# Kernel tuning notes

Hardware: AMD Instinct MI355X
Metric: run time of the kernel (lower is better)

Reference implementation:

```python
import jax, jax.numpy as jnp
import numpy as np

ALPHA = 0.2          # LeakyReLU negative slope (args.alpha)
NEG_INF = -9e15      # zero_vec constant from the torch source


def _build_mask(neighbors):
    """Faithful port of A_creat: scatter-add edge counts, row-normalize,
    add self-loops (identity), row-normalize again. neighbors: [N, deg] int."""
    N, deg = neighbors.shape
    rows = jnp.repeat(jnp.arange(N), deg)
    counts = jnp.zeros((N, N), jnp.float32).at[rows, neighbors.reshape(-1)].add(1.0)
    m = counts / counts.sum(axis=1, keepdims=True)
    m = m + jnp.eye(N, dtype=jnp.float32)
    m = m / m.sum(axis=1, keepdims=True)
    return m


def setup_inputs() -> dict:
    key = jax.random.key(0)
    k1, k2, k3, k4 = jax.random.split(key, 4)
    N, F_IN, F_OUT, DEG = 8192, 256, 128, 32
    h = jax.random.normal(k1, (N, F_IN), dtype=jnp.float32)
    neighbors = jax.random.randint(k2, (N, DEG), 0, N)
    # torch uses nn.init.uniform_ (U[0,1)) for both W and a
    W = jax.random.uniform(k3, (F_IN, F_OUT), dtype=jnp.float32)
    a = jax.random.uniform(k4, (2 * F_OUT, 1), dtype=jnp.float32)
    return {"h": h, "W": W, "a": a, "neighbors": neighbors}


def reference(h, W, a, neighbors):
    F_out = W.shape[1]
    mask = _build_mask(neighbors)                 # [N, N]
    hW = h @ W                                    # [N, F_out]
    h1 = hW @ a[:F_out]                           # [N, 1]
    h2 = hW @ a[F_out:]                           # [N, 1]
    e = mask * (h1 + h2.T)                        # dense masked additive scores
    e = jnp.where(e > 0, e, ALPHA * e)            # LeakyReLU
    att = jnp.where(e != 0.0, e, NEG_INF)         # mask out zeros
    att = jax.nn.softmax(att, axis=1)             # row softmax (dropout off in eval)
    feat = att @ hW                               # aggregate
    return jax.nn.elu(feat)
```

## Files before the change

### kernel.cpp

```cpp
#include <hip/hip_runtime.h>
#include <math.h>

#define N_NODES 8192
#define F_IN    256
#define F_OUT   128
#define DEG     32
#define ALPHA   0.2f

__global__ void gemm_hw_kernel(const float* __restrict__ h,
                               const float* __restrict__ W,
                               float* __restrict__ hW) {
    __shared__ float hs[8 * F_IN];
    const int tid  = threadIdx.x;
    const int row0 = blockIdx.x * 8;

    const float4* hsrc = (const float4*)(h + (size_t)row0 * F_IN);
    float4* hdst = (float4*)hs;
    #pragma unroll
    for (int t = 0; t < 4; ++t)
        hdst[tid + t * 128] = hsrc[tid + t * 128];
    __syncthreads();

    float acc[8] = {0.f, 0.f, 0.f, 0.f, 0.f, 0.f, 0.f, 0.f};
    #pragma unroll 4
    for (int k = 0; k < F_IN; ++k) {
        float w = W[k * F_OUT + tid];
        #pragma unroll
        for (int r = 0; r < 8; ++r)
            acc[r] = fmaf(hs[r * F_IN + k], w, acc[r]);
    }
    #pragma unroll
    for (int r = 0; r < 8; ++r)
        hW[(size_t)(row0 + r) * F_OUT + tid] = acc[r];
}

__global__ void h1h2_kernel(const float* __restrict__ hW,
                            const float* __restrict__ a,
                            float* __restrict__ h1,
                            float* __restrict__ h2) {
    const int wave = threadIdx.x >> 6;
    const int lane = threadIdx.x & 63;
    const int row  = blockIdx.x * 4 + wave;
    const float* hr = hW + (size_t)row * F_OUT;

    float s1 = 0.f, s2 = 0.f;
    #pragma unroll
    for (int j = lane; j < F_OUT; j += 64) {
        float v = hr[j];
        s1 = fmaf(v, a[j], s1);
        s2 = fmaf(v, a[F_OUT + j], s2);
    }
    #pragma unroll
    for (int off = 32; off > 0; off >>= 1) {
        s1 += __shfl_down(s1, off);
        s2 += __shfl_down(s2, off);
    }
    if (lane == 0) { h1[row] = s1; h2[row] = s2; }
}

__global__ void attn_kernel(const float* __restrict__ hW,
                            const float* __restrict__ h1,
                            const float* __restrict__ h2,
                            const int*   __restrict__ nbr,
                            float* __restrict__ out) {
    const int wave = threadIdx.x >> 6;
    const int lane = threadIdx.x & 63;
    const int row  = blockIdx.x * 4 + wave;

    int col = -1;
    if (lane < DEG)       col = nbr[(size_t)row * DEG + lane];
    else if (lane == DEG) col = row;

    int cnt = 0;
    int firstq = lane;
    #pragma unroll
    for (int q = 0; q <= DEG; ++q) {
        int cq = __shfl(col, q);
        bool same = (cq == col);
        if (same && q < DEG)    cnt++;
        if (same && q < firstq) firstq = q;
    }
    const bool active = (lane <= DEG) && (col >= 0) && (firstq == lane);

    float mask_val = (float)cnt * (1.0f / 64.0f) + ((col == row) ? 0.5f : 0.0f);

    const float h1row = h1[row];
    float h2c = active ? h2[col] : 0.f;
    float s = mask_val * (h1row + h2c);
    float e = (s > 0.f) ? s : ALPHA * s;
    bool valid = active && (e != 0.0f);

    float ev = valid ? e : -INFINITY;
    #pragma unroll
    for (int off = 32; off > 0; off >>= 1)
        ev = fmaxf(ev, __shfl_xor(ev, off));
    float w = valid ? expf(e - ev) : 0.f;
    float denom = w;
    #pragma unroll
    for (int off = 32; off > 0; off >>= 1)
        denom += __shfl_xor(denom, off);
    float att = w / denom;

    float acc0 = 0.f, acc1 = 0.f;
    #pragma unroll
    for (int q = 0; q <= DEG; ++q) {
        float aq = __shfl(att, q);
        int   cq = __shfl(col, q);
        if (aq > 0.f) {
            const float* hr = hW + (size_t)cq * F_OUT;
            acc0 = fmaf(aq, hr[lane],      acc0);
            acc1 = fmaf(aq, hr[64 + lane], acc1);
        }
    }

    float o0 = (acc0 > 0.f) ? acc0 : expm1f(acc0);
    float o1 = (acc1 > 0.f) ? acc1 : expm1f(acc1);
    out[(size_t)row * F_OUT + lane]      = o0;
    out[(size_t)row * F_OUT + 64 + lane] = o1;
}

extern "C" void kernel_launch(void* const* d_in, const int* in_sizes, int n_in,
                              void* d_out, int out_size, void* d_ws, size_t ws_size,
                              hipStream_t stream) {
    const float* h   = (const float*)d_in[0];
    const float* W   = (const float*)d_in[1];
    const float* a   = (const float*)d_in[2];
    const int*   nbr = (const int*)  d_in[3];
    float* out = (float*)d_out;

    float* hW = (float*)d_ws;
    float* h1 = hW + (size_t)N_NODES * F_OUT;
    float* h2 = h1 + N_NODES;

    gemm_hw_kernel<<<N_NODES / 8, 128, 0, stream>>>(h, W, hW);
    h1h2_kernel   <<<N_NODES / 4, 256, 0, stream>>>(hW, a, h1, h2);
    attn_kernel   <<<N_NODES / 4, 256, 0, stream>>>(hW, h1, h2, nbr, out);
}
```

Before: 102.8 us.

## Fuse attention-vector dot into a register-tiled GEMM and store hW as bf16

Replaces the naive hW GEMM with a 16-row register-tiled kernel. It double-buffers its LDS tiles, loading W asynchronously straight into LDS and staging h through registers. The h1/h2 projections are folded into the GEMM epilogue, which removes a separate kernel launch and a re-read of hW. hW is written as packed bf16 pairs, halving the gather traffic in the attention kernel, which also switches to fast __expf and vectorized float2 output stores. In exchange, the aggregated features lose precision because of the bf16 hW, and the GEMM grows more complex.

```diff
diff --git a/kernel.cpp b/kernel.cpp
--- a/kernel.cpp
+++ b/kernel.cpp
@@ -7,62 +7,133 @@
 #define DEG     32
 #define ALPHA   0.2f
 
-__global__ void gemm_hw_kernel(const float* __restrict__ h,
-                               const float* __restrict__ W,
-                               float* __restrict__ hW) {
-    __shared__ float hs[8 * F_IN];
+#define BR      16
+#define KC      32
+#define HP      36
+#define NCHUNK  (F_IN / KC)
+
+typedef const uint32_t __attribute__((address_space(1)))* gas_ptr;
+typedef uint32_t __attribute__((address_space(3)))* las_ptr;
+
+__device__ __forceinline__ void async_copy16(const float* g, float* l) {
+    __builtin_amdgcn_global_load_lds((gas_ptr)g, (las_ptr)l, 16, 0, 0);
+}
+
+__device__ __forceinline__ unsigned short f2bf(float x) {
+    unsigned u = __float_as_uint(x);
+    return (unsigned short)((u + 0x7fffu + ((u >> 16) & 1u)) >> 16);
+}
+
+__global__ __launch_bounds__(256) void gemm_fused_v4(
+        const float* __restrict__ h,
+        const float* __restrict__ W,
+        const float* __restrict__ a,
+        unsigned int* __restrict__ hWb,
+        float* __restrict__ h1,
+        float* __restrict__ h2) {
+    __shared__ float hT[2][BR * HP];
+    __shared__ float wT[2][KC * F_OUT];
+
     const int tid  = threadIdx.x;
-    const int row0 = blockIdx.x * 8;
-
-    const float4* hsrc = (const float4*)(h + (size_t)row0 * F_IN);
-    float4* hdst = (float4*)hs;
-    #pragma unroll
-    for (int t = 0; t < 4; ++t)
-        hdst[tid + t * 128] = hsrc[tid + t * 128];
+    const int wv   = tid >> 6;
+    const int lane = tid & 63;
+    const int cg   = tid & 31;
+    const int rg   = tid >> 5;
+    const int c0   = cg * 4;
+    const int r0   = rg * 2;
+    const int row0 = blockIdx.x * BR;
+
+    float acc[2][4] = {{0.f,0.f,0.f,0.f},{0.f,0.f,0.f,0.f}};
+
+    auto stage_w = [&](int k0, int buf) {
+        const float* gsrc = W + (size_t)k0 * F_OUT + wv * 1024 + lane * 4;
+        float*       ldst = wT[buf] + wv * 1024;
+        #pragma unroll
+        for (int it = 0; it < 4; ++it)
+            async_copy16(gsrc + it * 256, ldst + it * 256);
+    };
+    const int hrow = tid >> 3;
+    const int hkq  = (tid & 7) * 4;
+    auto load_h = [&](int k0) -> float4 {
+        if (tid < 128)
+            return *(const float4*)(h + (size_t)(row0 + hrow) * F_IN + k0 + hkq);
+        return make_float4(0.f, 0.f, 0.f, 0.f);
+    };
+    auto commit_h = [&](float4 v, int buf) {
+        if (tid < 128)
+            *(float4*)(hT[buf] + hrow * HP + hkq) = v;
+    };
+
+    stage_w(0, 0);
+    commit_h(load_h(0), 0);
     __syncthreads();
 
-    float acc[8] = {0.f, 0.f, 0.f, 0.f, 0.f, 0.f, 0.f, 0.f};
-    #pragma unroll 4
-    for (int k = 0; k < F_IN; ++k) {
-        float w = W[k * F_OUT + tid];
+    for (int ch = 0; ch < NCHUNK; ++ch) {
+        const int cur = ch & 1, nxt = cur ^ 1;
+        float4 hv_next;
+        if (ch + 1 < NCHUNK) {
+            stage_w((ch + 1) * KC, nxt);
+            hv_next = load_h((ch + 1) * KC);
+        }
+
+        const float* hc = hT[cur];
+        const float* wc = wT[cur];
         #pragma unroll
-        for (int r = 0; r < 8; ++r)
-            acc[r] = fmaf(hs[r * F_IN + k], w, acc[r]);
-    }
-    #pragma unroll
-    for (int r = 0; r < 8; ++r)
-        hW[(size_t)(row0 + r) * F_OUT + tid] = acc[r];
-}
-
-__global__ void h1h2_kernel(const float* __restrict__ hW,
-                            const float* __restrict__ a,
-                            float* __restrict__ h1,
-                            float* __restrict__ h2) {
-    const int wave = threadIdx.x >> 6;
-    const int lane = threadIdx.x & 63;
-    const int row  = blockIdx.x * 4 + wave;
-    const float* hr = hW + (size_t)row * F_OUT;
-
-    float s1 = 0.f, s2 = 0.f;
-    #pragma unroll
-    for (int j = lane; j < F_OUT; j += 64) {
-        float v = hr[j];
-        s1 = fmaf(v, a[j], s1);
-        s2 = fmaf(v, a[F_OUT + j], s2);
-    }
-    #pragma unroll
-    for (int off = 32; off > 0; off >>= 1) {
-        s1 += __shfl_down(s1, off);
-        s2 += __shfl_down(s2, off);
-    }
-    if (lane == 0) { h1[row] = s1; h2[row] = s2; }
-}
-
-__global__ void attn_kernel(const float* __restrict__ hW,
-                            const float* __restrict__ h1,
-                            const float* __restrict__ h2,
-                            const int*   __restrict__ nbr,
-                            float* __restrict__ out) {
+        for (int k4 = 0; k4 < KC; k4 += 4) {
+            float4 h0 = *(const float4*)(hc + (r0    ) * HP + k4);
+            float4 h1v= *(const float4*)(hc + (r0 + 1) * HP + k4);
+            const float h0a[4] = {h0.x, h0.y, h0.z, h0.w};
+            const float h1a[4] = {h1v.x, h1v.y, h1v.z, h1v.w};
+            #pragma unroll
+            for (int kk = 0; kk < 4; ++kk) {
+                float4 wvv = *(const float4*)(wc + (k4 + kk) * F_OUT + c0);
+                acc[0][0] = fmaf(h0a[kk], wvv.x, acc[0][0]);
+                acc[0][1] = fmaf(h0a[kk], wvv.y, acc[0][1]);
+                acc[0][2] = fmaf(h0a[kk], wvv.z, acc[0][2]);
+                acc[0][3] = fmaf(h0a[kk], wvv.w, acc[0][3]);
+                acc[1][0] = fmaf(h1a[kk], wvv.x, acc[1][0]);
+                acc[1][1] = fmaf(h1a[kk], wvv.y, acc[1][1]);
+                acc[1][2] = fmaf(h1a[kk], wvv.z, acc[1][2]);
+                acc[1][3] = fmaf(h1a[kk], wvv.w, acc[1][3]);
+            }
+        }
+
+        if (ch + 1 < NCHUNK) commit_h(hv_next, nxt);
+        __syncthreads();
+    }
+
+    #pragma unroll
+    for (int i = 0; i < 2; ++i) {
+        uint2 p;
+        p.x = (unsigned)f2bf(acc[i][0]) | ((unsigned)f2bf(acc[i][1]) << 16);
+        p.y = (unsigned)f2bf(acc[i][2]) | ((unsigned)f2bf(acc[i][3]) << 16);
+        *(uint2*)(hWb + (size_t)(row0 + r0 + i) * (F_OUT / 2) + c0 / 2) = p;
+    }
+
+    float4 a1 = *(const float4*)(a + c0);
+    float4 a2 = *(const float4*)(a + F_OUT + c0);
+    #pragma unroll
+    for (int i = 0; i < 2; ++i) {
+        float s1 = acc[i][0]*a1.x + acc[i][1]*a1.y + acc[i][2]*a1.z + acc[i][3]*a1.w;
+        float s2 = acc[i][0]*a2.x + acc[i][1]*a2.y + acc[i][2]*a2.z + acc[i][3]*a2.w;
+        #pragma unroll
+        for (int off = 1; off < 32; off <<= 1) {
+            s1 += __shfl_xor(s1, off);
+            s2 += __shfl_xor(s2, off);
+        }
+        if (cg == 0) {
+            h1[row0 + r0 + i] = s1;
+            h2[row0 + r0 + i] = s2;
+        }
+    }
+}
+
+__global__ __launch_bounds__(256) void attn_kernel(
+        const unsigned int* __restrict__ hWb,
+        const float* __restrict__ h1,
+        const float* __restrict__ h2,
+        const int*   __restrict__ nbr,
+        float* __restrict__ out) {
     const int wave = threadIdx.x >> 6;
     const int lane = threadIdx.x & 63;
     const int row  = blockIdx.x * 4 + wave;
@@ -94,7 +165,7 @@
     #pragma unroll
     for (int off = 32; off > 0; off >>= 1)
         ev = fmaxf(ev, __shfl_xor(ev, off));
-    float w = valid ? expf(e - ev) : 0.f;
+    float w = valid ? __expf(e - ev) : 0.f;
     float denom = w;
     #pragma unroll
     for (int off = 32; off > 0; off >>= 1)
@@ -107,16 +178,17 @@
         float aq = __shfl(att, q);
         int   cq = __shfl(col, q);
         if (aq > 0.f) {
-            const float* hr = hW + (size_t)cq * F_OUT;
-            acc0 = fmaf(aq, hr[lane],      acc0);
-            acc1 = fmaf(aq, hr[64 + lane], acc1);
+            unsigned v = hWb[(size_t)cq * (F_OUT / 2) + lane];
+            float lo = __uint_as_float(v << 16);
+            float hi = __uint_as_float(v & 0xffff0000u);
+            acc0 = fmaf(aq, lo, acc0);
+            acc1 = fmaf(aq, hi, acc1);
         }
     }
 
     float o0 = (acc0 > 0.f) ? acc0 : expm1f(acc0);
     float o1 = (acc1 > 0.f) ? acc1 : expm1f(acc1);
-    out[(size_t)row * F_OUT + lane]      = o0;
-    out[(size_t)row * F_OUT + 64 + lane] = o1;
+    *(float2*)(out + (size_t)row * F_OUT + 2 * lane) = make_float2(o0, o1);
 }
 
 extern "C" void kernel_launch(void* const* d_in, const int* in_sizes, int n_in,
@@ -128,11 +200,10 @@
     const int*   nbr = (const int*)  d_in[3];
     float* out = (float*)d_out;
 
-    float* hW = (float*)d_ws;
-    float* h1 = hW + (size_t)N_NODES * F_OUT;
+    unsigned int* hWb = (unsigned int*)d_ws;
+    float* h1 = (float*)(hWb + (size_t)N_NODES * (F_OUT / 2));
     float* h2 = h1 + N_NODES;
 
-    gemm_hw_kernel<<<N_NODES / 8, 128, 0, stream>>>(h, W, hW);
-    h1h2_kernel   <<<N_NODES / 4, 256, 0, stream>>>(hW, a, h1, h2);
-    attn_kernel   <<<N_NODES / 4, 256, 0, stream>>>(hW, h1, h2, nbr, out);
-}
+    gemm_fused_v4<<<N_NODES / BR, 256, 0, stream>>>(h, W, a, hWb, h1, h2);
+    attn_kernel  <<<N_NODES / 4,  256, 0, stream>>>(hWb, h1, h2, nbr, out);
+}
```

Result: faster. 94.21 us (-8.4%).
